# Optimization experiments

Hardware: AMD Instinct MI355X
Metric: run time of the kernel (lower is better)

## Reference

```python
import jax, jax.numpy as jnp
import numpy as np

T, B, Y, X, C = 9, 2, 128, 128, 64
W = (T - 1) // 2
WIN, HEADS = 8, 4
EPS = 1e-3  # keras LayerNormalization default epsilon


def _get_indices(center, size):
    right = list(range(center, size, 2))
    left = list(range(center - 2, -1, -2))
    idx = np.array(left[::-1] + right, dtype=np.int32)
    return np.clip(idx, 1, size - 2)


def _pyramid_indices(t):
    levels = []
    size, center = t, (t - 1) // 2
    while size > 1:
        c = _get_indices(center, size)
        levels.append((c - 1, c, c + 1))
        center = int(np.where(c == center)[0][0])
        size = len(c)
    return levels


LEVELS = _pyramid_indices(T)            # 3 levels for T=9: sizes 5, 3, 1
CIN = [C * (l + 1) for l in range(len(LEVELS))]    # 64, 128, 192
COUT = [C * (l + 2) for l in range(len(LEVELS))]   # 128, 192, 256


def _window_attention(q, kv, wqkv, bqkv, wo, bo):
    # WindowSpatialAttention: non-overlapping WINxWIN windows, MHA of q over kv.
    N, Yd, Xd, Cd = q.shape
    w, h = WIN, HEADS
    dh = Cd // h
    nY, nX = Yd // w, Xd // w

    def to_win(t):
        t = t.reshape(N, nY, w, nX, w, Cd).transpose(0, 1, 3, 2, 4, 5)
        return t.reshape(N * nY * nX, w * w, Cd)

    qw, kvw = to_win(q), to_win(kv)
    qp = (qw @ wqkv[0] + bqkv[0]).reshape(-1, w * w, h, dh)
    kp = (kvw @ wqkv[1] + bqkv[1]).reshape(-1, w * w, h, dh)
    vp = (kvw @ wqkv[2] + bqkv[2]).reshape(-1, w * w, h, dh)
    logits = jnp.einsum('nqhd,nkhd->nhqk', qp, kp) / jnp.sqrt(jnp.float32(dh))
    attn = jax.nn.softmax(logits, axis=-1)
    out = jnp.einsum('nhqk,nkhd->nqhd', attn, vp).reshape(-1, w * w, Cd)
    out = out @ wo + bo
    out = out.reshape(N, nY, nX, w, w, Cd).transpose(0, 1, 3, 2, 4, 5)
    return out.reshape(N, Yd, Xd, Cd)


def _forward(x, params):
    fidx = np.arange(T) - W  # relative frame indices, static (non frame-aware)
    current = x
    level1 = None
    for l, (pi, ci, ni) in enumerate(LEVELS):
        emb, lng, lnb, wqkv, bqkv, wo, bo, cw, cb = params[l]
        cin = current.shape[-1]
        # additive relative temporal embedding, indexed by frame offset + W
        t_emb = emb[fidx + W]                       # [Tl, cin]
        cur = current + t_emb[:, None, None, None, :]
        mu = cur.mean(-1, keepdims=True)
        var = cur.var(-1, keepdims=True)
        cur = (cur - mu) * jax.lax.rsqrt(var + EPS) * lng + lnb
        S = len(ci)
        prev = cur[pi].reshape(S * B, Y, X, cin)
        cen = cur[ci].reshape(S * B, Y, X, cin)
        nxt = cur[ni].reshape(S * B, Y, X, cin)
        q = jnp.concatenate([cen, prev, cen, nxt], axis=0)
        kv = jnp.concatenate([prev, cen, nxt, cen], axis=0)
        att = _window_attention(q, kv, wqkv, bqkv, wo, bo)
        parts = jnp.split(att, 4, axis=0)           # SplitBatch(n_splits=4)
        comb = jnp.concatenate(parts, axis=-1)      # Combine: concat + 1x1 conv
        down = jax.nn.relu(comb @ cw + cb)
        if S > 1:
            down = down.reshape(S, B, Y, X, down.shape[-1])
        if l == 0:
            level1 = down
        current = down
        fidx = fidx[ci]
    return current, level1


def setup_inputs() -> dict:
    key = jax.random.key(0)
    ks = iter(jax.random.split(key, 64))
    inp = {'x': jax.random.normal(next(ks), (T, B, Y, X, C), jnp.float32)}
    for l, (ci, co) in enumerate(zip(CIN, COUT)):
        inp[f'emb{l}'] = 0.02 * jax.random.normal(next(ks), (T, ci), jnp.float32)
        inp[f'lng{l}'] = jnp.ones((ci,), jnp.float32)
        inp[f'lnb{l}'] = jnp.zeros((ci,), jnp.float32)
        inp[f'wqkv{l}'] = 0.02 * jax.random.normal(next(ks), (3, ci, ci), jnp.float32)
        inp[f'bqkv{l}'] = jnp.zeros((3, ci), jnp.float32)
        inp[f'wo{l}'] = 0.02 * jax.random.normal(next(ks), (ci, ci), jnp.float32)
        inp[f'bo{l}'] = jnp.zeros((ci,), jnp.float32)
        inp[f'cw{l}'] = 0.02 * jax.random.normal(next(ks), (4 * ci, co), jnp.float32)
        inp[f'cb{l}'] = jnp.zeros((co,), jnp.float32)
    return inp


def reference(x, emb0, lng0, lnb0, wqkv0, bqkv0, wo0, bo0, cw0, cb0,
              emb1, lng1, lnb1, wqkv1, bqkv1, wo1, bo1, cw1, cb1,
              emb2, lng2, lnb2, wqkv2, bqkv2, wo2, bo2, cw2, cb2):
    params = [
        (emb0, lng0, lnb0, wqkv0, bqkv0, wo0, bo0, cw0, cb0),
        (emb1, lng1, lnb1, wqkv1, bqkv1, wo1, bo1, cw1, cb1),
        (emb2, lng2, lnb2, wqkv2, bqkv2, wo2, bo2, cw2, cb2),
    ]
    return _forward(x, params)
```

## Files before the change

kernel.cpp:

```cpp
#include <hip/hip_runtime.h>

typedef _Float16 f16;
typedef f16 f16x4 __attribute__((ext_vector_type(4)));
typedef f16 f16x8 __attribute__((ext_vector_type(8)));
typedef float f32x4 __attribute__((ext_vector_type(4)));

#define MFMA16(a, b, c) __builtin_amdgcn_mfma_f32_16x16x16f16((a), (b), (c), 0, 0, 0)
#define MFMA32(a, b, c) __builtin_amdgcn_mfma_f32_16x16x32_f16((a), (b), (c), 0, 0, 0)

struct Meta   { int pi[5], ci[5], ni[5]; };
struct EmbMap { int m[9]; };

template <int CIN>
__global__ __launch_bounds__(256) void ln_kernel(
    const float* in, long lda, const float* __restrict__ emb,
    const float* __restrict__ lng, const float* __restrict__ lnb,
    f16* out, long ldo, EmbMap em) {
  long row = (long)blockIdx.x * 4 + (threadIdx.x >> 6);
  int t = (int)(row >> 15);
  int lane = threadIdx.x & 63;
  constexpr int NCH = CIN / 64;
  const float* xr = in + row * lda;
  const float* er = emb + (long)em.m[t] * CIN;
  float v[NCH];
  float s = 0.f;
#pragma unroll
  for (int i = 0; i < NCH; ++i) { int c = lane + (i << 6); v[i] = xr[c] + er[c]; s += v[i]; }
#pragma unroll
  for (int o = 32; o >= 1; o >>= 1) s += __shfl_xor(s, o);
  float mu = s * (1.f / CIN), ss = 0.f;
#pragma unroll
  for (int i = 0; i < NCH; ++i) { float d = v[i] - mu; ss += d * d; }
#pragma unroll
  for (int o = 32; o >= 1; o >>= 1) ss += __shfl_xor(ss, o);
  float inv = rsqrtf(ss * (1.f / CIN) + 1e-3f);
  f16* orow = out + row * ldo;
#pragma unroll
  for (int i = 0; i < NCH; ++i) {
    int c = lane + (i << 6);
    orow[c] = (f16)((v[i] - mu) * inv * lng[c] + lnb[c]);
  }
}

template <int CIN>
__global__ __launch_bounds__(64) void wT_kernel(const float* __restrict__ wqkv,
                                                f16* __restrict__ wqkvT) {
  int j = blockIdx.x;
  int which = j / CIN, jj = j % CIN;
  const float* src = wqkv + (long)which * CIN * CIN + jj;
  f16* dst = wqkvT + (long)j * CIN;
  for (int c = threadIdx.x; c < CIN; c += 64) dst[c] = (f16)src[(long)c * CIN];
}

template <int CIN, int CO>
__global__ __launch_bounds__(256) void woc_kernel(
    const float* __restrict__ wo, const float* __restrict__ bo,
    const float* __restrict__ cw, const float* __restrict__ cb,
    f16* __restrict__ wocA, float* __restrict__ fb) {
  __shared__ float scw[4 * CIN];
  __shared__ float red[256];
  int o = blockIdx.x;
  for (int i = threadIdx.x; i < 4 * CIN; i += 256) scw[i] = cw[(long)i * CO + o];
  __syncthreads();
  for (int pm = threadIdx.x; pm < 4 * CIN; pm += 256) {
    int p = pm / CIN, mm = pm % CIN;
    const float* wr = wo + (long)mm * CIN;
    const float* sc = scw + p * CIN;
    float s = 0.f;
    for (int c = 0; c < CIN; ++c) s += wr[c] * sc[c];
    wocA[((long)(pm >> 3) * CO + o) * 8 + (pm & 7)] = (f16)s;
  }
  float part = 0.f;
  for (int i = threadIdx.x; i < 4 * CIN; i += 256) part += bo[i % CIN] * scw[i];
  red[threadIdx.x] = part;
  __syncthreads();
  for (int st = 128; st > 0; st >>= 1) {
    if (threadIdx.x < st) red[threadIdx.x] += red[threadIdx.x + st];
    __syncthreads();
  }
  if (threadIdx.x == 0) fb[o] = cb[o] + red[0];
}

template <int CIN>
__global__ __launch_bounds__(256) void proj_kernel(
    const f16* __restrict__ cur, long lda, const f16* __restrict__ wT,
    const float* __restrict__ bqkv, f16* __restrict__ gq, f16* __restrict__ gk,
    f16* __restrict__ gvt) {
  constexpr int KS = CIN / 32;
  constexpr int NT = CIN / 16;
  constexpr int C8 = CIN / 8;
  __shared__ f16 sB[CIN * CIN];
  int which = blockIdx.x;
  long win = blockIdx.y;
  long img = win >> 8;
  int wid = (int)(win & 255);
  int wy = wid >> 4, wx = wid & 15;
  int w = threadIdx.x >> 6, lane = threadIdx.x & 63;
  int r16 = lane & 15, kq = lane >> 4;

  int tok = w * 16 + r16;
  long orig = img * 16384 + (long)(wy * 8 + (tok >> 3)) * 128 + wx * 8 + (tok & 7);
  const f16* arow = cur + orig * lda + kq * 8;
  f16x8 a[KS];
#pragma unroll
  for (int ks = 0; ks < KS; ++ks) a[ks] = *(const f16x8*)(arow + ks * 32);

  const f16* wsrc = wT + (long)which * CIN * CIN;
  for (int idx = threadIdx.x; idx < CIN * C8; idx += 256) {
    int j = idx / C8, c8 = idx % C8;
    f16x8 v = *(const f16x8*)(wsrc + idx * 8);
    int off = ((j * CIN + c8 * 8) * 2) ^ ((j & 7) << 4);
    *(f16x8*)((char*)sB + off) = v;
  }
  __syncthreads();

  f32x4 acc[NT] = {};
#pragma unroll
  for (int ks = 0; ks < KS; ++ks) {
#pragma unroll
    for (int t = 0; t < NT; ++t) {
      int off = (((t * 16 + r16) * CIN + ks * 32 + kq * 8) * 2) ^ ((r16 & 7) << 4);
      f16x8 bb = *(const f16x8*)((char*)sB + off);
      acc[t] = MFMA32(a[ks], bb, acc[t]);
    }
  }
  __syncthreads();

  if (which < 2) {
#pragma unroll
    for (int t = 0; t < NT; ++t) {
      float bias = bqkv[which * CIN + t * 16 + r16];
#pragma unroll
      for (int rg = 0; rg < 4; ++rg) {
        int r = w * 16 + kq * 4 + rg;
        int c = t * 16 + r16;
        int off = ((r * CIN + c) * 2) ^ ((r & 7) << 4);
        *(f16*)((char*)sB + off) = (f16)(acc[t][rg] + bias);
      }
    }
    __syncthreads();
    f16* dst = (which ? gk : gq) + win * 64 * CIN;
    for (int idx = threadIdx.x; idx < 64 * C8; idx += 256) {
      int r = idx / C8, c8 = idx % C8;
      int off = ((r * CIN + c8 * 8) * 2) ^ ((r & 7) << 4);
      f16x8 v = *(const f16x8*)((char*)sB + off);
      *(f16x8*)(dst + r * CIN + c8 * 8) = v;
    }
  } else {
#pragma unroll
    for (int t = 0; t < NT; ++t) {
      float bias = bqkv[2 * CIN + t * 16 + r16];
#pragma unroll
      for (int rg = 0; rg < 4; ++rg) {
        int c = t * 16 + r16;
        int pos = w * 16 + kq * 4 + rg;
        int off = ((c * 64 + pos) * 2) ^ ((c & 7) << 4);
        *(f16*)((char*)sB + off) = (f16)(acc[t][rg] + bias);
      }
    }
    __syncthreads();
    for (int c = threadIdx.x; c < CIN; c += 256) {
      f16* dst = gvt + (win * CIN + c) * 64;
#pragma unroll
      for (int p8 = 0; p8 < 8; ++p8) {
        int off = ((c * 64 + p8 * 8) * 2) ^ ((c & 7) << 4);
        *(f16x8*)(dst + p8 * 8) = *(const f16x8*)((char*)sB + off);
      }
    }
  }
}

template <int CIN, int DH, int CO>
__global__ __launch_bounds__(256) void attn_kernel(
    const f16* __restrict__ gq, const f16* __restrict__ gk,
    const f16* __restrict__ gvt, const f16* __restrict__ wocA,
    const float* __restrict__ fb, float* __restrict__ out, Meta m) {
  constexpr int NKS = DH / 16;
  constexpr int NK8 = DH / 32;
  constexpr int NK4 = (DH % 32) / 16;
  constexpr int CO4 = CO / 4;
  constexpr int NTC = CO4 / 16;
  constexpr int NKD = CIN / 32;
  constexpr float scale = (DH == 16) ? 0.25f : (DH == 32) ? 0.1767766952966369f
                                                          : 0.1443375672974064f;
  constexpr float escale = scale * 1.4426950408889634f;
  __shared__ f16 O[2][64 * CIN];

  int img = blockIdx.y;
  int sidx = img >> 1, b = img & 1;
  int wid = blockIdx.x;
  int wy = wid >> 4, wx = wid & 15;
  int h = threadIdx.x >> 6, lane = threadIdx.x & 63;
  int r16 = lane & 15, kq = lane >> 4;
  int fpi = m.pi[sidx], fci = m.ci[sidx], fni = m.ni[sidx];

  f32x4 dn[NTC][4] = {};

#pragma unroll
  for (int p = 0; p < 4; ++p) {
    int qfr = (p == 1) ? fpi : ((p == 3) ? fni : fci);
    int kfr = (p == 0) ? fpi : ((p == 2) ? fni : fci);
    long qwin = (long)((qfr * 2 + b) * 256 + wid);
    long kwin = (long)((kfr * 2 + b) * 256 + wid);

    f16x8 kf8[4][NK8 ? NK8 : 1];
    f16x4 kf4[4][NK4 ? NK4 : 1];
#pragma unroll
    for (int tj = 0; tj < 4; ++tj) {
      const f16* kb = gk + (kwin * 64 + tj * 16 + r16) * CIN + h * DH;
      if constexpr (NK8 > 0)
#pragma unroll
        for (int n = 0; n < NK8; ++n)
          kf8[tj][n] = *(const f16x8*)(kb + n * 32 + kq * 8);
      if constexpr (NK4 > 0)
#pragma unroll
        for (int n = 0; n < NK4; ++n)
          kf4[tj][n] = *(const f16x4*)(kb + NK8 * 32 + n * 16 + kq * 4);
    }
    f16x4 va[NKS][4];
#pragma unroll
    for (int dt = 0; dt < NKS; ++dt)
#pragma unroll
      for (int jt = 0; jt < 4; ++jt)
        va[dt][jt] = *(const f16x4*)(gvt + (kwin * CIN + h * DH + dt * 16 + r16) * 64 +
                                     jt * 16 + kq * 4);

    f16x4 pa[4][4];
#pragma unroll
    for (int ti = 0; ti < 4; ++ti) {
      const f16* qb = gq + (qwin * 64 + ti * 16 + r16) * CIN + h * DH;
      f32x4 s4[4] = {};
      if constexpr (NK8 > 0) {
        f16x8 qf8[NK8];
#pragma unroll
        for (int n = 0; n < NK8; ++n) qf8[n] = *(const f16x8*)(qb + n * 32 + kq * 8);
#pragma unroll
        for (int tj = 0; tj < 4; ++tj)
#pragma unroll
          for (int n = 0; n < NK8; ++n) s4[tj] = MFMA32(kf8[tj][n], qf8[n], s4[tj]);
      }
      if constexpr (NK4 > 0) {
        f16x4 qf4[NK4];
#pragma unroll
        for (int n = 0; n < NK4; ++n)
          qf4[n] = *(const f16x4*)(qb + NK8 * 32 + n * 16 + kq * 4);
#pragma unroll
        for (int tj = 0; tj < 4; ++tj)
#pragma unroll
          for (int n = 0; n < NK4; ++n) s4[tj] = MFMA16(kf4[tj][n], qf4[n], s4[tj]);
      }
      float sum = 0.f;
#pragma unroll
      for (int tj = 0; tj < 4; ++tj)
#pragma unroll
        for (int rg = 0; rg < 4; ++rg) {
          float e = __builtin_amdgcn_exp2f(s4[tj][rg] * escale);
          s4[tj][rg] = e;
          sum += e;
        }
      sum += __shfl_xor(sum, 16);
      sum += __shfl_xor(sum, 32);
      float inv = 1.f / sum;
#pragma unroll
      for (int tj = 0; tj < 4; ++tj) {
        f16x4 pv;
#pragma unroll
        for (int rg = 0; rg < 4; ++rg) pv[rg] = (f16)(s4[tj][rg] * inv);
        pa[tj][ti] = pv;
      }
    }

    char* Ob = (char*)O[p & 1];
#pragma unroll
    for (int dt = 0; dt < NKS; ++dt) {
#pragma unroll
      for (int ti = 0; ti < 4; ++ti) {
        f32x4 po = {};
#pragma unroll
        for (int jt = 0; jt < 4; ++jt) po = MFMA16(va[dt][jt], pa[jt][ti], po);
        int i = ti * 16 + r16;
        int c0 = h * DH + dt * 16 + kq * 4;
        f16x4 pk;
#pragma unroll
        for (int rg = 0; rg < 4; ++rg) pk[rg] = (f16)po[rg];
        int off = ((i * CIN + c0) * 2) ^ ((i & 7) << 4);
        *(f16x4*)(Ob + off) = pk;
      }
    }
    __syncthreads();

#pragma unroll
    for (int ck = 0; ck < NKD; ++ck) {
      f16x8 ob[4];
#pragma unroll
      for (int ti = 0; ti < 4; ++ti) {
        int i = ti * 16 + r16;
        int off = ((i * CIN + ck * 32 + kq * 8) * 2) ^ ((i & 7) << 4);
        ob[ti] = *(const f16x8*)(Ob + off);
      }
      long pm = (long)(p * CIN + ck * 32 + kq * 8);
#pragma unroll
      for (int ot = 0; ot < NTC; ++ot) {
        f16x8 wa = *(const f16x8*)(wocA + ((pm >> 3) * CO + h * CO4 + ot * 16 + r16) * 8);
#pragma unroll
        for (int ti = 0; ti < 4; ++ti) dn[ot][ti] = MFMA32(wa, ob[ti], dn[ot][ti]);
      }
    }
  }

#pragma unroll
  for (int ot = 0; ot < NTC; ++ot) {
    f32x4 fb4 = *(const f32x4*)(fb + h * CO4 + ot * 16 + kq * 4);
#pragma unroll
    for (int ti = 0; ti < 4; ++ti) {
      int i = ti * 16 + r16;
      long gtok = (long)img * 16384 + (wy * 8 + (i >> 3)) * 128 + wx * 8 + (i & 7);
      f32x4 v;
#pragma unroll
      for (int rg = 0; rg < 4; ++rg) v[rg] = fmaxf(dn[ot][ti][rg] + fb4[rg], 0.f);
      *(f32x4*)(out + gtok * CO + h * CO4 + ot * 16 + kq * 4) = v;
    }
  }
}

extern "C" void kernel_launch(void* const* d_in, const int* in_sizes, int n_in,
                              void* d_out, int out_size, void* d_ws, size_t ws_size,
                              hipStream_t stream) {
  const float* x = (const float*)d_in[0];
#define PRM(l, k) ((const float*)d_in[1 + 9 * (l) + (k)])
  float* outCur = (float*)d_out;
  float* outL1 = (float*)d_out + 8388608;

  char* ws = (char*)d_ws;
  const size_t OFF_B = 125829120ull;
  const size_t OFF_W = OFF_B + 75497472ull;
  f16* qkvbase = (f16*)ws;
  char* wsB = ws + OFF_B;
  float* accum1 = (float*)wsB;
  f16* wqkvT = (f16*)(ws + OFF_W);
  f16* wocA = (f16*)(ws + OFF_W + 262144);
  float* fb = (float*)(ws + OFF_W + 262144 + 524288);

  Meta m0 = {{0, 1, 3, 5, 6}, {1, 2, 4, 6, 7}, {2, 3, 5, 7, 8}};
  Meta m1 = {{0, 1, 2, 0, 0}, {1, 2, 3, 0, 0}, {2, 3, 4, 0, 0}};
  Meta m2 = {{0, 0, 0, 0, 0}, {1, 0, 0, 0, 0}, {2, 0, 0, 0, 0}};
  EmbMap em0 = {{0, 1, 2, 3, 4, 5, 6, 7, 8}};
  EmbMap em1 = {{1, 2, 4, 6, 7, 0, 0, 0, 0}};
  EmbMap em2 = {{2, 4, 6, 0, 0, 0, 0, 0, 0}};

  {
    constexpr int CIN = 64, DH = 16, CO = 128, TL = 9, S = 5;
    long ntok = (long)TL * 2 * 16384;
    f16 *gq = qkvbase, *gk = gq + ntok * CIN, *gvt = gk + ntok * CIN;
    f16* cur = (f16*)wsB;
    ln_kernel<CIN><<<dim3((unsigned)(ntok / 4)), 256, 0, stream>>>(
        x, CIN, PRM(0, 0), PRM(0, 1), PRM(0, 2), cur, CIN, em0);
    wT_kernel<CIN><<<dim3(3 * CIN), 64, 0, stream>>>(PRM(0, 3), wqkvT);
    woc_kernel<CIN, CO><<<dim3(CO), 256, 0, stream>>>(PRM(0, 5), PRM(0, 6), PRM(0, 7), PRM(0, 8), wocA, fb);
    proj_kernel<CIN><<<dim3(3, (unsigned)(ntok / 64)), 256, 0, stream>>>(
        cur, CIN, wqkvT, PRM(0, 4), gq, gk, gvt);
    attn_kernel<CIN, DH, CO><<<dim3(256, S * 2), 256, 0, stream>>>(
        gq, gk, gvt, wocA, fb, outL1, m0);
  }
  {
    constexpr int CIN = 128, DH = 32, CO = 192, TL = 5, S = 3;
    long ntok = (long)TL * 2 * 16384;
    f16 *gq = qkvbase, *gk = gq + ntok * CIN, *gvt = gk + ntok * CIN;
    f16* cur = (f16*)wsB;
    ln_kernel<CIN><<<dim3((unsigned)(ntok / 4)), 256, 0, stream>>>(
        outL1, CIN, PRM(1, 0), PRM(1, 1), PRM(1, 2), cur, CIN, em1);
    wT_kernel<CIN><<<dim3(3 * CIN), 64, 0, stream>>>(PRM(1, 3), wqkvT);
    woc_kernel<CIN, CO><<<dim3(CO), 256, 0, stream>>>(PRM(1, 5), PRM(1, 6), PRM(1, 7), PRM(1, 8), wocA, fb);
    proj_kernel<CIN><<<dim3(3, (unsigned)(ntok / 64)), 256, 0, stream>>>(
        cur, CIN, wqkvT, PRM(1, 4), gq, gk, gvt);
    attn_kernel<CIN, DH, CO><<<dim3(256, S * 2), 256, 0, stream>>>(
        gq, gk, gvt, wocA, fb, accum1, m1);
  }
  {
    constexpr int CIN = 192, DH = 48, CO = 256, TL = 3, S = 1;
    long ntok = (long)TL * 2 * 16384;
    f16 *gq = qkvbase, *gk = gq + ntok * CIN, *gvt = gk + ntok * CIN;
    f16* cur = (f16*)accum1;
    ln_kernel<CIN><<<dim3((unsigned)(ntok / 4)), 256, 0, stream>>>(
        accum1, CIN, PRM(2, 0), PRM(2, 1), PRM(2, 2), cur, 384, em2);
    wT_kernel<CIN><<<dim3(3 * CIN), 64, 0, stream>>>(PRM(2, 3), wqkvT);
    woc_kernel<CIN, CO><<<dim3(CO), 256, 0, stream>>>(PRM(2, 5), PRM(2, 6), PRM(2, 7), PRM(2, 8), wocA, fb);
    proj_kernel<CIN><<<dim3(3, (unsigned)(ntok / 64)), 256, 0, stream>>>(
        cur, 384, wqkvT, PRM(2, 4), gq, gk, gvt);
    attn_kernel<CIN, DH, CO><<<dim3(256, S * 2), 256, 0, stream>>>(
        gq, gk, gvt, wocA, fb, outCur, m2);
  }
#undef PRM
}
```

Measured before the change: 629.8 us.

## Add attn4 kernel assigning one wave per attention pair for levels 0 and 1

Adds a new attention kernel in which each of the four waves computes one of the four query/key frame pairings for every head, storing its output in its own LDS buffer. All four buffers are then concatenated along the reduction dimension for the fused output projection and conv matmul. This changes how work is split across waves, likely away from the old kernel's two-buffer scheme, and is meant to raise parallelism and remove serialization inside the block. It doubles LDS use (4×64×CIN f16), which may lower occupancy, especially at CIN=128. Level 2 keeps the old kernel.

```diff
diff --git a/kernel.cpp b/kernel.cpp
--- a/kernel.cpp
+++ b/kernel.cpp
@@ -171,6 +171,162 @@
 }
 
 template <int CIN, int DH, int CO>
+__global__ __launch_bounds__(256) void attn4_kernel(
+    const f16* __restrict__ gq, const f16* __restrict__ gk,
+    const f16* __restrict__ gvt, const f16* __restrict__ wocA,
+    const float* __restrict__ fb, float* __restrict__ out, Meta m) {
+  constexpr int NKS = DH / 16;
+  constexpr int NK8 = DH / 32;
+  constexpr int NK4 = (DH % 32) / 16;
+  constexpr int CO4 = CO / 4;
+  constexpr int NTC = CO4 / 16;
+  constexpr int NKD = 4 * CIN / 32;
+  constexpr float scale = (DH == 16) ? 0.25f : (DH == 32) ? 0.1767766952966369f
+                                                          : 0.1443375672974064f;
+  constexpr float escale = scale * 1.4426950408889634f;
+  __shared__ f16 O[4][64 * CIN];
+
+  int img = blockIdx.y;
+  int sidx = img >> 1, b = img & 1;
+  int wid = blockIdx.x;
+  int wy = wid >> 4, wx = wid & 15;
+  int p = threadIdx.x >> 6, lane = threadIdx.x & 63;
+  int r16 = lane & 15, kq = lane >> 4;
+  int fpi = m.pi[sidx], fci = m.ci[sidx], fni = m.ni[sidx];
+
+  int qfr = (p == 1) ? fpi : ((p == 3) ? fni : fci);
+  int kfr = (p == 0) ? fpi : ((p == 2) ? fni : fci);
+  long qwin = (long)((qfr * 2 + b) * 256 + wid);
+  long kwin = (long)((kfr * 2 + b) * 256 + wid);
+  char* Ob = (char*)O[p];
+
+#pragma unroll
+  for (int hh = 0; hh < 4; ++hh) {
+    f16x8 kf8[4][NK8 ? NK8 : 1];
+    f16x4 kf4[4][NK4 ? NK4 : 1];
+#pragma unroll
+    for (int tj = 0; tj < 4; ++tj) {
+      const f16* kb = gk + (kwin * 64 + tj * 16 + r16) * CIN + hh * DH;
+      if constexpr (NK8 > 0)
+#pragma unroll
+        for (int n = 0; n < NK8; ++n)
+          kf8[tj][n] = *(const f16x8*)(kb + n * 32 + kq * 8);
+      if constexpr (NK4 > 0)
+#pragma unroll
+        for (int n = 0; n < NK4; ++n)
+          kf4[tj][n] = *(const f16x4*)(kb + NK8 * 32 + n * 16 + kq * 4);
+    }
+    f16x4 va[NKS][4];
+#pragma unroll
+    for (int dt = 0; dt < NKS; ++dt)
+#pragma unroll
+      for (int jt = 0; jt < 4; ++jt)
+        va[dt][jt] = *(const f16x4*)(gvt + (kwin * CIN + hh * DH + dt * 16 + r16) * 64 +
+                                     jt * 16 + kq * 4);
+
+    f16x4 pa[4][4];
+#pragma unroll
+    for (int ti = 0; ti < 4; ++ti) {
+      const f16* qb = gq + (qwin * 64 + ti * 16 + r16) * CIN + hh * DH;
+      f32x4 s4[4] = {};
+      if constexpr (NK8 > 0) {
+        f16x8 qf8[NK8];
+#pragma unroll
+        for (int n = 0; n < NK8; ++n) qf8[n] = *(const f16x8*)(qb + n * 32 + kq * 8);
+#pragma unroll
+        for (int tj = 0; tj < 4; ++tj)
+#pragma unroll
+          for (int n = 0; n < NK8; ++n) s4[tj] = MFMA32(kf8[tj][n], qf8[n], s4[tj]);
+      }
+      if constexpr (NK4 > 0) {
+        f16x4 qf4[NK4];
+#pragma unroll
+        for (int n = 0; n < NK4; ++n)
+          qf4[n] = *(const f16x4*)(qb + NK8 * 32 + n * 16 + kq * 4);
+#pragma unroll
+        for (int tj = 0; tj < 4; ++tj)
+#pragma unroll
+          for (int n = 0; n < NK4; ++n) s4[tj] = MFMA16(kf4[tj][n], qf4[n], s4[tj]);
+      }
+      float sum = 0.f;
+#pragma unroll
+      for (int tj = 0; tj < 4; ++tj)
+#pragma unroll
+        for (int rg = 0; rg < 4; ++rg) {
+          float e = __builtin_amdgcn_exp2f(s4[tj][rg] * escale);
+          s4[tj][rg] = e;
+          sum += e;
+        }
+      sum += __shfl_xor(sum, 16);
+      sum += __shfl_xor(sum, 32);
+      float inv = 1.f / sum;
+#pragma unroll
+      for (int tj = 0; tj < 4; ++tj) {
+        f16x4 pv;
+#pragma unroll
+        for (int rg = 0; rg < 4; ++rg) pv[rg] = (f16)(s4[tj][rg] * inv);
+        pa[tj][ti] = pv;
+      }
+    }
+
+#pragma unroll
+    for (int dt = 0; dt < NKS; ++dt) {
+#pragma unroll
+      for (int ti = 0; ti < 4; ++ti) {
+        f32x4 po = {};
+#pragma unroll
+        for (int jt = 0; jt < 4; ++jt) po = MFMA16(va[dt][jt], pa[jt][ti], po);
+        int i = ti * 16 + r16;
+        int c0 = hh * DH + dt * 16 + kq * 4;
+        f16x4 pk;
+#pragma unroll
+        for (int rg = 0; rg < 4; ++rg) pk[rg] = (f16)po[rg];
+        int off = ((i * CIN + c0) * 2) ^ ((i & 7) << 4);
+        *(f16x4*)(Ob + off) = pk;
+      }
+    }
+  }
+  __syncthreads();
+
+  f32x4 dn[NTC][4] = {};
+#pragma unroll
+  for (int ck = 0; ck < NKD; ++ck) {
+    int k0 = ck * 32;
+    int psrc = k0 / CIN;
+    int c = k0 - psrc * CIN;
+    char* Osrc = (char*)O[psrc];
+    f16x8 ob[4];
+#pragma unroll
+    for (int ti = 0; ti < 4; ++ti) {
+      int i = ti * 16 + r16;
+      int off = ((i * CIN + c + kq * 8) * 2) ^ ((i & 7) << 4);
+      ob[ti] = *(const f16x8*)(Osrc + off);
+    }
+    long pm = (long)(k0 + kq * 8);
+#pragma unroll
+    for (int ot = 0; ot < NTC; ++ot) {
+      f16x8 wa = *(const f16x8*)(wocA + ((pm >> 3) * CO + p * CO4 + ot * 16 + r16) * 8);
+#pragma unroll
+      for (int ti = 0; ti < 4; ++ti) dn[ot][ti] = MFMA32(wa, ob[ti], dn[ot][ti]);
+    }
+  }
+
+#pragma unroll
+  for (int ot = 0; ot < NTC; ++ot) {
+    f32x4 fb4 = *(const f32x4*)(fb + p * CO4 + ot * 16 + kq * 4);
+#pragma unroll
+    for (int ti = 0; ti < 4; ++ti) {
+      int i = ti * 16 + r16;
+      long gtok = (long)img * 16384 + (wy * 8 + (i >> 3)) * 128 + wx * 8 + (i & 7);
+      f32x4 v;
+#pragma unroll
+      for (int rg = 0; rg < 4; ++rg) v[rg] = fmaxf(dn[ot][ti][rg] + fb4[rg], 0.f);
+      *(f32x4*)(out + gtok * CO + p * CO4 + ot * 16 + kq * 4) = v;
+    }
+  }
+}
+
+template <int CIN, int DH, int CO>
 __global__ __launch_bounds__(256) void attn_kernel(
     const f16* __restrict__ gq, const f16* __restrict__ gk,
     const f16* __restrict__ gvt, const f16* __restrict__ wocA,
@@ -359,7 +515,7 @@
     woc_kernel<CIN, CO><<<dim3(CO), 256, 0, stream>>>(PRM(0, 5), PRM(0, 6), PRM(0, 7), PRM(0, 8), wocA, fb);
     proj_kernel<CIN><<<dim3(3, (unsigned)(ntok / 64)), 256, 0, stream>>>(
         cur, CIN, wqkvT, PRM(0, 4), gq, gk, gvt);
-    attn_kernel<CIN, DH, CO><<<dim3(256, S * 2), 256, 0, stream>>>(
+    attn4_kernel<CIN, DH, CO><<<dim3(256, S * 2), 256, 0, stream>>>(
         gq, gk, gvt, wocA, fb, outL1, m0);
   }
   {
@@ -373,7 +529,7 @@
     woc_kernel<CIN, CO><<<dim3(CO), 256, 0, stream>>>(PRM(1, 5), PRM(1, 6), PRM(1, 7), PRM(1, 8), wocA, fb);
     proj_kernel<CIN><<<dim3(3, (unsigned)(ntok / 64)), 256, 0, stream>>>(
         cur, CIN, wqkvT, PRM(1, 4), gq, gk, gvt);
-    attn_kernel<CIN, DH, CO><<<dim3(256, S * 2), 256, 0, stream>>>(
+    attn4_kernel<CIN, DH, CO><<<dim3(256, S * 2), 256, 0, stream>>>(
         gq, gk, gvt, wocA, fb, accum1, m1);
   }
   {
```

New measurement: 656.4 us. 4.2% more time.
